# Optimization experiments

Hardware: AMD Instinct MI355X
Metric: run time of the kernel (lower is better)

Reference implementation:

```python
import jax, jax.numpy as jnp
import numpy as np

N = 16384
DIM_IN = 128
DIM_OUT = 128
HIDDEN = (DIM_IN + DIM_OUT) // 2  # 128


def setup_inputs() -> dict:
    key = jax.random.key(0)
    ks = jax.random.split(key, 8)
    s_in = 1.0 / np.sqrt(DIM_IN)
    s_h = 1.0 / np.sqrt(HIDDEN)
    return {
        "x": jax.random.normal(ks[0], (N, DIM_IN), dtype=jnp.float32),
        "adj": jax.random.uniform(ks[1], (N, N), dtype=jnp.float32) * (1.0 / N),
        "W2": jax.random.uniform(ks[2], (DIM_IN, HIDDEN), minval=-s_in, maxval=s_in, dtype=jnp.float32),
        "b2": jnp.zeros((HIDDEN,), dtype=jnp.float32),
        "W4": jax.random.uniform(ks[3], (HIDDEN, DIM_OUT), minval=-s_h, maxval=s_h, dtype=jnp.float32),
        "b4": jnp.zeros((DIM_OUT,), dtype=jnp.float32),
        "res_w": jax.random.uniform(ks[4], (DIM_OUT, HIDDEN), minval=-s_h, maxval=s_h, dtype=jnp.float32),
        "res_b": jax.random.uniform(ks[5], (DIM_OUT,), minval=-s_h, maxval=s_h, dtype=jnp.float32),
    }


def gcn(x, adj, W, b):
    # GraphConvolution: support = x @ W; out = adj @ support + b
    return adj @ (x @ W) + b


def reference(x, adj, W2, b2, W4, b4, res_w, res_b):
    local_hidden = gcn(x, adj, W2, b2)          # [N, HIDDEN]
    local_cross = gcn(local_hidden, adj, W4, b4)  # [N, DIM_OUT]
    # addRes: residual linear projection of local_hidden
    embed = local_cross + local_hidden @ res_w.T + res_b
    return embed
```

## Files before the change

kernel.cpp:

```cpp
#include <hip/hip_runtime.h>
#include <hip/hip_bf16.h>

#define MN 16384
#define SPLITS 4
#define KSLICE (MN / SPLITS)
#define BK 64
#define NSTEPS (KSLICE / BK)
#define NSUPER (NSTEPS / 2)

typedef float f32x4 __attribute__((ext_vector_type(4)));
typedef int   i32x4 __attribute__((ext_vector_type(4)));

#define A8S 32768.0f
#define SB1 64.0f
#define SB2 4096.0f
#define SC1 (1.0f / (32768.0f * 64.0f))
#define SC2 (1.0f / (32768.0f * 4096.0f))

__device__ __forceinline__ void async16(void* lds, const void* g) {
  __builtin_amdgcn_global_load_lds(
      (const __attribute__((address_space(1))) unsigned int*)g,
      (__attribute__((address_space(3))) unsigned int*)lds, 16, 0, 0);
}


__global__ __launch_bounds__(256)
void k1_xw2(const float* __restrict__ x, const float* __restrict__ W2,
            unsigned char* __restrict__ B1) {
  __shared__ __align__(16) float xs[64 * 128];
  const int t = threadIdx.x;
  const long rowbase = (long)blockIdx.x * 64;
  const f32x4* xg = (const f32x4*)(x + rowbase * 128);
  f32x4* xl = (f32x4*)xs;
#pragma unroll
  for (int i = 0; i < 8; ++i) xl[t + 256 * i] = xg[t + 256 * i];
  __syncthreads();
  const int r0 = (t >> 5) * 8;
  const int c0 = (t & 31) * 4;
  float acc[8][4] = {};
  for (int k = 0; k < 128; k += 4) {
    f32x4 w[4];
#pragma unroll
    for (int kk = 0; kk < 4; ++kk) w[kk] = *(const f32x4*)(W2 + (k + kk) * 128 + c0);
#pragma unroll
    for (int i = 0; i < 8; ++i) {
      f32x4 xv = *(const f32x4*)(xs + (r0 + i) * 128 + k);
#pragma unroll
      for (int kk = 0; kk < 4; ++kk)
#pragma unroll
        for (int j = 0; j < 4; ++j) acc[i][j] += xv[kk] * w[kk][j];
    }
  }
  const long U = (rowbase + r0) >> 3;
  i32x4 wv0, wv1;
#pragma unroll
  for (int j = 0; j < 4; ++j) {
    int lo = __builtin_amdgcn_cvt_pk_fp8_f32(acc[0][j] * SB1, acc[1][j] * SB1, 0, false);
    lo     = __builtin_amdgcn_cvt_pk_fp8_f32(acc[2][j] * SB1, acc[3][j] * SB1, lo, true);
    int hi = __builtin_amdgcn_cvt_pk_fp8_f32(acc[4][j] * SB1, acc[5][j] * SB1, 0, false);
    hi     = __builtin_amdgcn_cvt_pk_fp8_f32(acc[6][j] * SB1, acc[7][j] * SB1, hi, true);
    if (j < 2) { wv0[2 * j] = lo; wv0[2 * j + 1] = hi; }
    else       { wv1[2 * (j - 2)] = lo; wv1[2 * (j - 2) + 1] = hi; }
  }
  *(i32x4*)(B1 + (U * 128 + c0) * 8)      = wv0;
  *(i32x4*)(B1 + (U * 128 + c0) * 8 + 16) = wv1;
}

template <int AMODE>
__global__ __launch_bounds__(256, 4)
void big_mm(const float* __restrict__ A, const unsigned char* __restrict__ A8r,
            unsigned char* __restrict__ A8w, const unsigned char* __restrict__ B8,
            float sc, float* __restrict__ P) {
  __shared__ __align__(16) unsigned char Bs[2][16384];
  const int tid  = threadIdx.x;
  const int wid  = tid >> 6;
  const int lane = tid & 63;
  const int g    = lane >> 4;
  const int cl   = lane & 15;
  const int tile_m = blockIdx.x & 255;
  const int s      = blockIdx.x >> 8;
  const long k0 = (long)s * KSLICE;

  const char* bsrc = (const char*)B8 + k0 * 128 + (long)tid * 16;
  const float* aptr = nullptr;
  if constexpr (AMODE != 1)
    aptr = A + (long)(tile_m * 64 + wid * 16 + cl) * MN + k0 + 16 * g;
  const long c8base = (long)blockIdx.x * (64L * 4096) + (long)tid * 16;

  f32x4 acc[8] = {};

  {
    unsigned char* d = &Bs[0][0] + wid * 1024;
    async16(d, bsrc);                 async16(d + 4096, bsrc + 4096);
    async16(d + 8192, bsrc + 8192);   async16(d + 12288, bsrc + 12288);
  }
  f32x4 a0n, a1n, a2n, a3n;
  i32x4 q8n;
  if constexpr (AMODE == 1) {
    q8n = *(const i32x4*)(A8r + c8base);
  } else {
    a0n = *(const f32x4*)aptr;       a1n = *(const f32x4*)(aptr + 4);
    a2n = *(const f32x4*)(aptr + 8); a3n = *(const f32x4*)(aptr + 12);
  }
  __syncthreads();

  for (int m = 0; m < NSUPER; ++m) {
    if (m + 1 < NSUPER) {
      unsigned char* d = &Bs[(m + 1) & 1][0] + wid * 1024;
      const char* src = bsrc + (long)(2 * m + 2) * 8192;
      async16(d, src);                 async16(d + 4096, src + 4096);
      async16(d + 8192, src + 8192);   async16(d + 12288, src + 12288);
    }
    __builtin_amdgcn_sched_barrier(0);

#pragma unroll
    for (int h = 0; h < 2; ++h) {
      const int t = 2 * m + h;
      int pk0, pk1, pk2, pk3;
      if constexpr (AMODE == 1) {
        i32x4 q8 = q8n;
        if (t + 1 < NSTEPS)
          q8n = *(const i32x4*)(A8r + c8base + (long)(t + 1) * 4096);
        pk0 = q8[0]; pk1 = q8[1]; pk2 = q8[2]; pk3 = q8[3];
      } else {
        f32x4 a0 = a0n, a1 = a1n, a2 = a2n, a3 = a3n;
        if (t + 1 < NSTEPS) {
          const float* ap = aptr + (long)(t + 1) * BK;
          a0n = *(const f32x4*)ap;       a1n = *(const f32x4*)(ap + 4);
          a2n = *(const f32x4*)(ap + 8); a3n = *(const f32x4*)(ap + 12);
        }
        pk0 = __builtin_amdgcn_cvt_pk_fp8_f32(a0[0] * A8S, a0[1] * A8S, 0, false);
        pk0 = __builtin_amdgcn_cvt_pk_fp8_f32(a0[2] * A8S, a0[3] * A8S, pk0, true);
        pk1 = __builtin_amdgcn_cvt_pk_fp8_f32(a1[0] * A8S, a1[1] * A8S, 0, false);
        pk1 = __builtin_amdgcn_cvt_pk_fp8_f32(a1[2] * A8S, a1[3] * A8S, pk1, true);
        pk2 = __builtin_amdgcn_cvt_pk_fp8_f32(a2[0] * A8S, a2[1] * A8S, 0, false);
        pk2 = __builtin_amdgcn_cvt_pk_fp8_f32(a2[2] * A8S, a2[3] * A8S, pk2, true);
        pk3 = __builtin_amdgcn_cvt_pk_fp8_f32(a3[0] * A8S, a3[1] * A8S, 0, false);
        pk3 = __builtin_amdgcn_cvt_pk_fp8_f32(a3[2] * A8S, a3[3] * A8S, pk3, true);
        if constexpr (AMODE == 0) {
          i32x4 st = {pk0, pk1, pk2, pk3};
          __builtin_nontemporal_store(st, (i32x4*)(A8w + c8base + (long)t * 4096));
        }
      }
      const long alo = ((long)(unsigned)pk1 << 32) | (unsigned)pk0;
      const long ahi = ((long)(unsigned)pk3 << 32) | (unsigned)pk2;

      const char* bb = (const char*)&Bs[m & 1][0] + h * 8192 + g * 2048 + cl * 8;
#pragma unroll
      for (int c = 0; c < 8; ++c) {
        long b0 = *(const long*)(bb + c * 128);
        long b1 = *(const long*)(bb + 1024 + c * 128);
        acc[c] = __builtin_amdgcn_mfma_f32_16x16x32_fp8_fp8(alo, b0, acc[c], 0, 0, 0);
        acc[c] = __builtin_amdgcn_mfma_f32_16x16x32_fp8_fp8(ahi, b1, acc[c], 0, 0, 0);
      }
    }

    if (m + 1 < NSUPER) {
      if constexpr (AMODE == 0)      asm volatile("s_waitcnt vmcnt(10)" ::: "memory");
      else if constexpr (AMODE == 2) asm volatile("s_waitcnt vmcnt(8)" ::: "memory");
      else                           asm volatile("s_waitcnt vmcnt(2)" ::: "memory");
      __builtin_amdgcn_s_barrier();
    }
  }

  float* pb = P + ((long)s * MN + tile_m * 64 + wid * 16) * 128;
#pragma unroll
  for (int c = 0; c < 8; ++c)
#pragma unroll
    for (int q = 0; q < 4; ++q)
      __builtin_nontemporal_store(acc[c][q] * sc,
                                  &pb[(g * 4 + q) * 128 + 16 * c + cl]);
}

__global__ __launch_bounds__(256)
void k3_mid(const float* __restrict__ P, const float* __restrict__ b2,
            const float* __restrict__ W4, const float* __restrict__ res_w,
            const float* __restrict__ b4, const float* __restrict__ res_b,
            unsigned char* __restrict__ B2, float* __restrict__ Rr) {
  __shared__ __align__(16) float hs[64 * 128];
  const int t = threadIdx.x;
  const long rowbase = (long)blockIdx.x * 64;
  const long base = rowbase * 32;
  const f32x4* P0 = (const f32x4*)P + base;
  const f32x4* P1 = (const f32x4*)P + (long)MN * 32 + base;
  const f32x4* P2 = (const f32x4*)P + 2L * MN * 32 + base;
  const f32x4* P3 = (const f32x4*)P + 3L * MN * 32 + base;
  const f32x4* b2v = (const f32x4*)b2;
  f32x4* hl = (f32x4*)hs;
#pragma unroll
  for (int i = 0; i < 8; ++i) {
    int idx = t + 256 * i;
    f32x4 v = __builtin_nontemporal_load(P0 + idx);
    v += __builtin_nontemporal_load(P1 + idx);
    v += __builtin_nontemporal_load(P2 + idx);
    v += __builtin_nontemporal_load(P3 + idx);
    hl[idx] = v + b2v[idx & 31];
  }
  __syncthreads();
  const int r0 = (t >> 5) * 8;
  const int c0 = (t & 31) * 4;
  float acc2[8][4] = {};
  float accR[8][4] = {};
  for (int k = 0; k < 128; k += 4) {
    f32x4 w4v[4], rwv[4];
#pragma unroll
    for (int kk = 0; kk < 4; ++kk) w4v[kk] = *(const f32x4*)(W4 + (k + kk) * 128 + c0);
#pragma unroll
    for (int j = 0; j < 4; ++j) rwv[j] = *(const f32x4*)(res_w + (c0 + j) * 128 + k);
#pragma unroll
    for (int i = 0; i < 8; ++i) {
      f32x4 xv = *(const f32x4*)(hs + (r0 + i) * 128 + k);
#pragma unroll
      for (int kk = 0; kk < 4; ++kk)
#pragma unroll
        for (int j = 0; j < 4; ++j) {
          acc2[i][j] += xv[kk] * w4v[kk][j];
          accR[i][j] += xv[kk] * rwv[j][kk];
        }
    }
  }
  const long U = (rowbase + r0) >> 3;
  i32x4 wv0, wv1;
#pragma unroll
  for (int j = 0; j < 4; ++j) {
    int lo = __builtin_amdgcn_cvt_pk_fp8_f32(acc2[0][j] * SB2, acc2[1][j] * SB2, 0, false);
    lo     = __builtin_amdgcn_cvt_pk_fp8_f32(acc2[2][j] * SB2, acc2[3][j] * SB2, lo, true);
    int hi = __builtin_amdgcn_cvt_pk_fp8_f32(acc2[4][j] * SB2, acc2[5][j] * SB2, 0, false);
    hi     = __builtin_amdgcn_cvt_pk_fp8_f32(acc2[6][j] * SB2, acc2[7][j] * SB2, hi, true);
    if (j < 2) { wv0[2 * j] = lo; wv0[2 * j + 1] = hi; }
    else       { wv1[2 * (j - 2)] = lo; wv1[2 * (j - 2) + 1] = hi; }
  }
  *(i32x4*)(B2 + (U * 128 + c0) * 8)      = wv0;
  *(i32x4*)(B2 + (U * 128 + c0) * 8 + 16) = wv1;

  const f32x4 b4v = *(const f32x4*)(b4 + c0);
  const f32x4 rbv = *(const f32x4*)(res_b + c0);
#pragma unroll
  for (int i = 0; i < 8; ++i) {
    f32x4 rv;
#pragma unroll
    for (int j = 0; j < 4; ++j) rv[j] = accR[i][j];
    rv += b4v + rbv;
    *(f32x4*)(Rr + (rowbase + r0 + i) * 128 + c0) = rv;
  }
}

__global__ __launch_bounds__(256)
void k5_out(const float* __restrict__ P, const float* __restrict__ Rr,
            float* __restrict__ out) {
  const long i = (long)blockIdx.x * 256 + threadIdx.x;
  const f32x4* P0 = (const f32x4*)P;
  const f32x4* P1 = P0 + (long)MN * 32;
  const f32x4* P2 = P0 + 2L * MN * 32;
  const f32x4* P3 = P0 + 3L * MN * 32;
  f32x4 v = __builtin_nontemporal_load(P0 + i);
  v += __builtin_nontemporal_load(P1 + i);
  v += __builtin_nontemporal_load(P2 + i);
  v += __builtin_nontemporal_load(P3 + i);
  v += *((const f32x4*)Rr + i);
  __builtin_nontemporal_store(v, (f32x4*)out + i);
}

extern "C" void kernel_launch(void* const* d_in, const int* in_sizes, int n_in,
                              void* d_out, int out_size, void* d_ws, size_t ws_size,
                              hipStream_t stream) {
  const float* x     = (const float*)d_in[0];
  const float* adj   = (const float*)d_in[1];
  const float* W2    = (const float*)d_in[2];
  const float* b2    = (const float*)d_in[3];
  const float* W4    = (const float*)d_in[4];
  const float* b4    = (const float*)d_in[5];
  const float* res_w = (const float*)d_in[6];
  const float* res_b = (const float*)d_in[7];
  float* out = (float*)d_out;

  char* ws = (char*)d_ws;
  unsigned char* B1 = (unsigned char*)ws;
  unsigned char* B2 = (unsigned char*)(ws + (4L << 20));
  float* Rr = (float*)(ws + (8L << 20));
  float* P  = (float*)(ws + (16L << 20));
  unsigned char* A8 = (unsigned char*)(ws + (48L << 20));

  const size_t need = (48L << 20) + (size_t)MN * MN;
  const bool fp8_copy = ws_size >= need;

  k1_xw2<<<dim3(256), dim3(256), 0, stream>>>(x, W2, B1);
  if (fp8_copy) {
    big_mm<0><<<dim3(256 * SPLITS), dim3(256), 0, stream>>>(adj, nullptr, A8, B1, SC1, P);
    k3_mid<<<dim3(256), dim3(256), 0, stream>>>(P, b2, W4, res_w, b4, res_b, B2, Rr);
    big_mm<1><<<dim3(256 * SPLITS), dim3(256), 0, stream>>>(nullptr, A8, nullptr, B2, SC2, P);
  } else {
    big_mm<2><<<dim3(256 * SPLITS), dim3(256), 0, stream>>>(adj, nullptr, nullptr, B1, SC1, P);
    k3_mid<<<dim3(256), dim3(256), 0, stream>>>(P, b2, W4, res_w, b4, res_b, B2, Rr);
    big_mm<2><<<dim3(256 * SPLITS), dim3(256), 0, stream>>>(adj, nullptr, nullptr, B2, SC2, P);
  }
  k5_out<<<dim3(2048), dim3(256), 0, stream>>>(P, Rr, out);
}
```

Measured before the change: 429.9 us.

## Use 1024-thread blocks holding the whole B slice in LDS, with fp8 split-K partials

Restructures big_mm so each 1024-thread block loads its entire 128KB B k-slice into LDS once and covers 256 rows. The 16 waves walk the k-steps in staggered order, which removes the double-buffered pipeline and its per-step barriers. The split count rises from 4 to 16, and the partial sums are stored as fp8 bytes instead of fp32, then dequantized and summed in k3_mid and k5_out. The aim is fewer barriers and less partial-sum traffic. The cost is extra fp8 rounding error on the partials, byte-granular scattered stores, and only one 128KB-LDS block resident per CU.

```diff
diff --git a/kernel.cpp b/kernel.cpp
--- a/kernel.cpp
+++ b/kernel.cpp
@@ -2,20 +2,24 @@
 #include <hip/hip_bf16.h>
 
 #define MN 16384
-#define SPLITS 4
+#define SPLITS 16
 #define KSLICE (MN / SPLITS)
 #define BK 64
 #define NSTEPS (KSLICE / BK)
-#define NSUPER (NSTEPS / 2)
+#define TROWS 256
+#define PSLICE (MN * 128L)
 
 typedef float f32x4 __attribute__((ext_vector_type(4)));
+typedef float f32x2 __attribute__((ext_vector_type(2)));
 typedef int   i32x4 __attribute__((ext_vector_type(4)));
 
-#define A8S 32768.0f
-#define SB1 64.0f
-#define SB2 4096.0f
-#define SC1 (1.0f / (32768.0f * 64.0f))
-#define SC2 (1.0f / (32768.0f * 4096.0f))
+#define A8S  32768.0f
+#define SB1  64.0f
+#define SB2  4096.0f
+#define F1ST 0.0078125f
+#define F2ST 0.001953125f
+#define K3SC (1.0f / 16384.0f)
+#define K5SC (1.0f / 262144.0f)
 
 __device__ __forceinline__ void async16(void* lds, const void* g) {
   __builtin_amdgcn_global_load_lds(
@@ -67,134 +71,130 @@
 }
 
 template <int AMODE>
-__global__ __launch_bounds__(256, 4)
+__global__ __launch_bounds__(1024, 4)
 void big_mm(const float* __restrict__ A, const unsigned char* __restrict__ A8r,
             unsigned char* __restrict__ A8w, const unsigned char* __restrict__ B8,
-            float sc, float* __restrict__ P) {
-  __shared__ __align__(16) unsigned char Bs[2][16384];
+            float fstore, unsigned char* __restrict__ P8) {
+  __shared__ __align__(16) unsigned char Bs[131072];
   const int tid  = threadIdx.x;
   const int wid  = tid >> 6;
   const int lane = tid & 63;
   const int g    = lane >> 4;
   const int cl   = lane & 15;
-  const int tile_m = blockIdx.x & 255;
-  const int s      = blockIdx.x >> 8;
+  const int tile_m = blockIdx.x & 63;
+  const int s      = blockIdx.x >> 6;
   const long k0 = (long)s * KSLICE;
 
-  const char* bsrc = (const char*)B8 + k0 * 128 + (long)tid * 16;
+  {
+    const char* src = (const char*)B8 + (long)s * 131072 +
+                      (long)wid * 1024 + (long)lane * 16;
+    unsigned char* dst = Bs + wid * 1024;
+#pragma unroll
+    for (int r = 0; r < 8; ++r)
+      async16(dst + r * 16384, src + (long)r * 16384);
+  }
+
+  const int row = tile_m * TROWS + wid * 16 + cl;
   const float* aptr = nullptr;
-  if constexpr (AMODE != 1)
-    aptr = A + (long)(tile_m * 64 + wid * 16 + cl) * MN + k0 + 16 * g;
-  const long c8base = (long)blockIdx.x * (64L * 4096) + (long)tid * 16;
+  if constexpr (AMODE != 1) aptr = A + (long)row * MN + k0 + 16 * g;
+  const long c8base = (long)blockIdx.x * (NSTEPS * 16384L) + (long)tid * 16;
 
   f32x4 acc[8] = {};
 
-  {
-    unsigned char* d = &Bs[0][0] + wid * 1024;
-    async16(d, bsrc);                 async16(d + 4096, bsrc + 4096);
-    async16(d + 8192, bsrc + 8192);   async16(d + 12288, bsrc + 12288);
-  }
-  f32x4 a0n, a1n, a2n, a3n;
-  i32x4 q8n;
+  f32x4 ab[2][4];
+  i32x4 qb[2];
   if constexpr (AMODE == 1) {
-    q8n = *(const i32x4*)(A8r + c8base);
+    qb[0] = *(const i32x4*)(A8r + c8base + (long)(wid & 15) * 16384);
+    qb[1] = *(const i32x4*)(A8r + c8base + (long)((wid + 1) & 15) * 16384);
   } else {
-    a0n = *(const f32x4*)aptr;       a1n = *(const f32x4*)(aptr + 4);
-    a2n = *(const f32x4*)(aptr + 8); a3n = *(const f32x4*)(aptr + 12);
+    const float* p0 = aptr + (long)(wid & 15) * BK;
+    const float* p1 = aptr + (long)((wid + 1) & 15) * BK;
+#pragma unroll
+    for (int j = 0; j < 4; ++j) {
+      ab[0][j] = *(const f32x4*)(p0 + 4 * j);
+      ab[1][j] = *(const f32x4*)(p1 + 4 * j);
+    }
   }
   __syncthreads();
 
-  for (int m = 0; m < NSUPER; ++m) {
-    if (m + 1 < NSUPER) {
-      unsigned char* d = &Bs[(m + 1) & 1][0] + wid * 1024;
-      const char* src = bsrc + (long)(2 * m + 2) * 8192;
-      async16(d, src);                 async16(d + 4096, src + 4096);
-      async16(d + 8192, src + 8192);   async16(d + 12288, src + 12288);
-    }
-    __builtin_amdgcn_sched_barrier(0);
-
-#pragma unroll
-    for (int h = 0; h < 2; ++h) {
-      const int t = 2 * m + h;
-      int pk0, pk1, pk2, pk3;
-      if constexpr (AMODE == 1) {
-        i32x4 q8 = q8n;
-        if (t + 1 < NSTEPS)
-          q8n = *(const i32x4*)(A8r + c8base + (long)(t + 1) * 4096);
-        pk0 = q8[0]; pk1 = q8[1]; pk2 = q8[2]; pk3 = q8[3];
-      } else {
-        f32x4 a0 = a0n, a1 = a1n, a2 = a2n, a3 = a3n;
-        if (t + 1 < NSTEPS) {
-          const float* ap = aptr + (long)(t + 1) * BK;
-          a0n = *(const f32x4*)ap;       a1n = *(const f32x4*)(ap + 4);
-          a2n = *(const f32x4*)(ap + 8); a3n = *(const f32x4*)(ap + 12);
-        }
-        pk0 = __builtin_amdgcn_cvt_pk_fp8_f32(a0[0] * A8S, a0[1] * A8S, 0, false);
-        pk0 = __builtin_amdgcn_cvt_pk_fp8_f32(a0[2] * A8S, a0[3] * A8S, pk0, true);
-        pk1 = __builtin_amdgcn_cvt_pk_fp8_f32(a1[0] * A8S, a1[1] * A8S, 0, false);
-        pk1 = __builtin_amdgcn_cvt_pk_fp8_f32(a1[2] * A8S, a1[3] * A8S, pk1, true);
-        pk2 = __builtin_amdgcn_cvt_pk_fp8_f32(a2[0] * A8S, a2[1] * A8S, 0, false);
-        pk2 = __builtin_amdgcn_cvt_pk_fp8_f32(a2[2] * A8S, a2[3] * A8S, pk2, true);
-        pk3 = __builtin_amdgcn_cvt_pk_fp8_f32(a3[0] * A8S, a3[1] * A8S, 0, false);
-        pk3 = __builtin_amdgcn_cvt_pk_fp8_f32(a3[2] * A8S, a3[3] * A8S, pk3, true);
-        if constexpr (AMODE == 0) {
-          i32x4 st = {pk0, pk1, pk2, pk3};
-          __builtin_nontemporal_store(st, (i32x4*)(A8w + c8base + (long)t * 4096));
-        }
+#pragma unroll
+  for (int i = 0; i < NSTEPS; ++i) {
+    const int t = (wid + i) & 15;
+    int pk0, pk1, pk2, pk3;
+    if constexpr (AMODE == 1) {
+      i32x4 q = qb[i & 1];
+      if (i + 2 < NSTEPS)
+        qb[i & 1] = *(const i32x4*)(A8r + c8base + (long)((wid + i + 2) & 15) * 16384);
+      pk0 = q[0]; pk1 = q[1]; pk2 = q[2]; pk3 = q[3];
+    } else {
+      f32x4 a0 = ab[i & 1][0], a1 = ab[i & 1][1], a2 = ab[i & 1][2], a3 = ab[i & 1][3];
+      if (i + 2 < NSTEPS) {
+        const float* ap = aptr + (long)((wid + i + 2) & 15) * BK;
+#pragma unroll
+        for (int j = 0; j < 4; ++j) ab[i & 1][j] = *(const f32x4*)(ap + 4 * j);
       }
-      const long alo = ((long)(unsigned)pk1 << 32) | (unsigned)pk0;
-      const long ahi = ((long)(unsigned)pk3 << 32) | (unsigned)pk2;
-
-      const char* bb = (const char*)&Bs[m & 1][0] + h * 8192 + g * 2048 + cl * 8;
-#pragma unroll
-      for (int c = 0; c < 8; ++c) {
-        long b0 = *(const long*)(bb + c * 128);
-        long b1 = *(const long*)(bb + 1024 + c * 128);
-        acc[c] = __builtin_amdgcn_mfma_f32_16x16x32_fp8_fp8(alo, b0, acc[c], 0, 0, 0);
-        acc[c] = __builtin_amdgcn_mfma_f32_16x16x32_fp8_fp8(ahi, b1, acc[c], 0, 0, 0);
+      pk0 = __builtin_amdgcn_cvt_pk_fp8_f32(a0[0] * A8S, a0[1] * A8S, 0, false);
+      pk0 = __builtin_amdgcn_cvt_pk_fp8_f32(a0[2] * A8S, a0[3] * A8S, pk0, true);
+      pk1 = __builtin_amdgcn_cvt_pk_fp8_f32(a1[0] * A8S, a1[1] * A8S, 0, false);
+      pk1 = __builtin_amdgcn_cvt_pk_fp8_f32(a1[2] * A8S, a1[3] * A8S, pk1, true);
+      pk2 = __builtin_amdgcn_cvt_pk_fp8_f32(a2[0] * A8S, a2[1] * A8S, 0, false);
+      pk2 = __builtin_amdgcn_cvt_pk_fp8_f32(a2[2] * A8S, a2[3] * A8S, pk2, true);
+      pk3 = __builtin_amdgcn_cvt_pk_fp8_f32(a3[0] * A8S, a3[1] * A8S, 0, false);
+      pk3 = __builtin_amdgcn_cvt_pk_fp8_f32(a3[2] * A8S, a3[3] * A8S, pk3, true);
+      if constexpr (AMODE == 0) {
+        i32x4 st = {pk0, pk1, pk2, pk3};
+        *(i32x4*)(A8w + c8base + (long)t * 16384) = st;
       }
     }
-
-    if (m + 1 < NSUPER) {
-      if constexpr (AMODE == 0)      asm volatile("s_waitcnt vmcnt(10)" ::: "memory");
-      else if constexpr (AMODE == 2) asm volatile("s_waitcnt vmcnt(8)" ::: "memory");
-      else                           asm volatile("s_waitcnt vmcnt(2)" ::: "memory");
-      __builtin_amdgcn_s_barrier();
-    }
-  }
-
-  float* pb = P + ((long)s * MN + tile_m * 64 + wid * 16) * 128;
-#pragma unroll
-  for (int c = 0; c < 8; ++c)
+    const long alo = ((long)(unsigned)pk1 << 32) | (unsigned)pk0;
+    const long ahi = ((long)(unsigned)pk3 << 32) | (unsigned)pk2;
+
+    const char* bb = (const char*)Bs + t * 8192 + g * 2048 + cl * 8;
+#pragma unroll
+    for (int c = 0; c < 8; ++c) {
+      long b0 = *(const long*)(bb + c * 128);
+      long b1 = *(const long*)(bb + 1024 + c * 128);
+      acc[c] = __builtin_amdgcn_mfma_f32_16x16x32_fp8_fp8(alo, b0, acc[c], 0, 0, 0);
+      acc[c] = __builtin_amdgcn_mfma_f32_16x16x32_fp8_fp8(ahi, b1, acc[c], 0, 0, 0);
+    }
+  }
+
+  unsigned char* pb = P8 + (long)s * PSLICE +
+                      (long)(tile_m * TROWS + wid * 16) * 128 + cl;
+#pragma unroll
+  for (int c = 0; c < 8; ++c) {
+    int w0 = __builtin_amdgcn_cvt_pk_fp8_f32(acc[c][0] * fstore, acc[c][1] * fstore, 0, false);
+    w0     = __builtin_amdgcn_cvt_pk_fp8_f32(acc[c][2] * fstore, acc[c][3] * fstore, w0, true);
 #pragma unroll
     for (int q = 0; q < 4; ++q)
-      __builtin_nontemporal_store(acc[c][q] * sc,
-                                  &pb[(g * 4 + q) * 128 + 16 * c + cl]);
+      __builtin_nontemporal_store((unsigned char)(((unsigned)w0) >> (8 * q)),
+                                  pb + (g * 4 + q) * 128 + 16 * c);
+  }
 }
 
 __global__ __launch_bounds__(256)
-void k3_mid(const float* __restrict__ P, const float* __restrict__ b2,
+void k3_mid(const unsigned char* __restrict__ P8, const float* __restrict__ b2,
             const float* __restrict__ W4, const float* __restrict__ res_w,
             const float* __restrict__ b4, const float* __restrict__ res_b,
             unsigned char* __restrict__ B2, float* __restrict__ Rr) {
   __shared__ __align__(16) float hs[64 * 128];
   const int t = threadIdx.x;
   const long rowbase = (long)blockIdx.x * 64;
-  const long base = rowbase * 32;
-  const f32x4* P0 = (const f32x4*)P + base;
-  const f32x4* P1 = (const f32x4*)P + (long)MN * 32 + base;
-  const f32x4* P2 = (const f32x4*)P + 2L * MN * 32 + base;
-  const f32x4* P3 = (const f32x4*)P + 3L * MN * 32 + base;
   const f32x4* b2v = (const f32x4*)b2;
   f32x4* hl = (f32x4*)hs;
 #pragma unroll
   for (int i = 0; i < 8; ++i) {
-    int idx = t + 256 * i;
-    f32x4 v = __builtin_nontemporal_load(P0 + idx);
-    v += __builtin_nontemporal_load(P1 + idx);
-    v += __builtin_nontemporal_load(P2 + idx);
-    v += __builtin_nontemporal_load(P3 + idx);
-    hl[idx] = v + b2v[idx & 31];
+    const int idx = t + 256 * i;
+    const unsigned char* pp = P8 + rowbase * 128 + (long)idx * 4;
+    f32x4 v = {};
+#pragma unroll
+    for (int sl = 0; sl < SPLITS; ++sl) {
+      unsigned q = *(const unsigned*)(pp + (long)sl * PSLICE);
+      f32x2 lo = __builtin_amdgcn_cvt_pk_f32_fp8(q, false);
+      f32x2 hi = __builtin_amdgcn_cvt_pk_f32_fp8(q, true);
+      v[0] += lo[0]; v[1] += lo[1]; v[2] += hi[0]; v[3] += hi[1];
+    }
+    hl[idx] = v * K3SC + b2v[idx & 31];
   }
   __syncthreads();
   const int r0 = (t >> 5) * 8;
@@ -246,18 +246,19 @@
 }
 
 __global__ __launch_bounds__(256)
-void k5_out(const float* __restrict__ P, const float* __restrict__ Rr,
+void k5_out(const unsigned char* __restrict__ P8, const float* __restrict__ Rr,
             float* __restrict__ out) {
   const long i = (long)blockIdx.x * 256 + threadIdx.x;
-  const f32x4* P0 = (const f32x4*)P;
-  const f32x4* P1 = P0 + (long)MN * 32;
-  const f32x4* P2 = P0 + 2L * MN * 32;
-  const f32x4* P3 = P0 + 3L * MN * 32;
-  f32x4 v = __builtin_nontemporal_load(P0 + i);
-  v += __builtin_nontemporal_load(P1 + i);
-  v += __builtin_nontemporal_load(P2 + i);
-  v += __builtin_nontemporal_load(P3 + i);
-  v += *((const f32x4*)Rr + i);
+  const unsigned char* pp = P8 + i * 4;
+  f32x4 v = {};
+#pragma unroll
+  for (int sl = 0; sl < SPLITS; ++sl) {
+    unsigned q = *(const unsigned*)(pp + (long)sl * PSLICE);
+    f32x2 lo = __builtin_amdgcn_cvt_pk_f32_fp8(q, false);
+    f32x2 hi = __builtin_amdgcn_cvt_pk_f32_fp8(q, true);
+    v[0] += lo[0]; v[1] += lo[1]; v[2] += hi[0]; v[3] += hi[1];
+  }
+  v = v * K5SC + *((const f32x4*)Rr + i);
   __builtin_nontemporal_store(v, (f32x4*)out + i);
 }
 
@@ -275,24 +276,25 @@
   float* out = (float*)d_out;
 
   char* ws = (char*)d_ws;
-  unsigned char* B1 = (unsigned char*)ws;
-  unsigned char* B2 = (unsigned char*)(ws + (4L << 20));
-  float* Rr = (float*)(ws + (8L << 20));
-  float* P  = (float*)(ws + (16L << 20));
-  unsigned char* A8 = (unsigned char*)(ws + (48L << 20));
-
-  const size_t need = (48L << 20) + (size_t)MN * MN;
+  unsigned char* P8 = (unsigned char*)ws;
+  unsigned char* B1 = (unsigned char*)(ws + (32L << 20));
+  unsigned char* B2 = (unsigned char*)(ws + (34L << 20));
+  float* Rr = (float*)(ws + (36L << 20));
+  unsigned char* A8 = (unsigned char*)(ws + (44L << 20));
+
+  const size_t need = (44L << 20) + (size_t)MN * MN;
   const bool fp8_copy = ws_size >= need;
 
+  const int BIGGRID = SPLITS * (MN / TROWS);
   k1_xw2<<<dim3(256), dim3(256), 0, stream>>>(x, W2, B1);
   if (fp8_copy) {
-    big_mm<0><<<dim3(256 * SPLITS), dim3(256), 0, stream>>>(adj, nullptr, A8, B1, SC1, P);
-    k3_mid<<<dim3(256), dim3(256), 0, stream>>>(P, b2, W4, res_w, b4, res_b, B2, Rr);
-    big_mm<1><<<dim3(256 * SPLITS), dim3(256), 0, stream>>>(nullptr, A8, nullptr, B2, SC2, P);
+    big_mm<0><<<dim3(BIGGRID), dim3(1024), 0, stream>>>(adj, nullptr, A8, B1, F1ST, P8);
+    k3_mid<<<dim3(256), dim3(256), 0, stream>>>(P8, b2, W4, res_w, b4, res_b, B2, Rr);
+    big_mm<1><<<dim3(BIGGRID), dim3(1024), 0, stream>>>(nullptr, A8, nullptr, B2, F2ST, P8);
   } else {
-    big_mm<2><<<dim3(256 * SPLITS), dim3(256), 0, stream>>>(adj, nullptr, nullptr, B1, SC1, P);
-    k3_mid<<<dim3(256), dim3(256), 0, stream>>>(P, b2, W4, res_w, b4, res_b, B2, Rr);
-    big_mm<2><<<dim3(256 * SPLITS), dim3(256), 0, stream>>>(adj, nullptr, nullptr, B2, SC2, P);
-  }
-  k5_out<<<dim3(2048), dim3(256), 0, stream>>>(P, Rr, out);
-}
+    big_mm<2><<<dim3(BIGGRID), dim3(1024), 0, stream>>>(adj, nullptr, nullptr, B1, F1ST, P8);
+    k3_mid<<<dim3(256), dim3(256), 0, stream>>>(P8, b2, W4, res_w, b4, res_b, B2, Rr);
+    big_mm<2><<<dim3(BIGGRID), dim3(1024), 0, stream>>>(adj, nullptr, nullptr, B2, F2ST, P8);
+  }
+  k5_out<<<dim3(2048), dim3(256), 0, stream>>>(P8, Rr, out);
+}
```

After: 497.7 us. +15.8%, slower.

## Stage fp32 adjacency tiles through swizzled LDS with async loads, 128-row blocks

Applied to the files above, without the earlier changes.

The big adjacency matmul now uses 512-thread blocks covering 128 rows each, which halves the grid. The fp32 A tile is streamed into a double-buffered, XOR-swizzled LDS region with async global-to-LDS loads instead of direct register loads. The loop is flattened to single 64-wide k-steps with one barrier per step, and the B staging shrinks to one 8KB buffer per step. The aim is to get wider, better-coalesced A reads that overlap with MFMA work. The cost is 80KB of LDS per block, which lowers occupancy, plus twice as many barriers.

```diff
diff --git a/kernel.cpp b/kernel.cpp
--- a/kernel.cpp
+++ b/kernel.cpp
@@ -6,7 +6,6 @@
 #define KSLICE (MN / SPLITS)
 #define BK 64
 #define NSTEPS (KSLICE / BK)
-#define NSUPER (NSTEPS / 2)
 
 typedef float f32x4 __attribute__((ext_vector_type(4)));
 typedef int   i32x4 __attribute__((ext_vector_type(4)));
@@ -67,103 +66,111 @@
 }
 
 template <int AMODE>
-__global__ __launch_bounds__(256, 4)
+__global__ __launch_bounds__(512, 4)
 void big_mm(const float* __restrict__ A, const unsigned char* __restrict__ A8r,
             unsigned char* __restrict__ A8w, const unsigned char* __restrict__ B8,
             float sc, float* __restrict__ P) {
-  __shared__ __align__(16) unsigned char Bs[2][16384];
+  constexpr int LDSSZ = (AMODE == 1) ? 16384 : 81920;
+  __shared__ __align__(16) unsigned char LB[LDSSZ];
   const int tid  = threadIdx.x;
   const int wid  = tid >> 6;
   const int lane = tid & 63;
   const int g    = lane >> 4;
   const int cl   = lane & 15;
-  const int tile_m = blockIdx.x & 255;
-  const int s      = blockIdx.x >> 8;
+  const int tile_m = blockIdx.x & 127;
+  const int s      = blockIdx.x >> 7;
   const long k0 = (long)s * KSLICE;
 
   const char* bsrc = (const char*)B8 + k0 * 128 + (long)tid * 16;
-  const float* aptr = nullptr;
-  if constexpr (AMODE != 1)
-    aptr = A + (long)(tile_m * 64 + wid * 16 + cl) * MN + k0 + 16 * g;
-  const long c8base = (long)blockIdx.x * (64L * 4096) + (long)tid * 16;
+  const long c8base = (long)blockIdx.x * (64L * 8192) + (long)tid * 16;
+
+  const char* asrc[4];
+  int aoff[4];
+  if constexpr (AMODE != 1) {
+    const int rl = lane >> 4;
+#pragma unroll
+    for (int q = 0; q < 4; ++q) {
+      const int row_local = wid * 16 + q * 4 + rl;
+      const int piece = ((lane & 15) * 16) ^ ((row_local & 7) << 4);
+      asrc[q] = (const char*)A + ((long)(tile_m * 128 + row_local) * MN + k0) * 4 + piece;
+    }
+    const int row = wid * 16 + cl;
+#pragma unroll
+    for (int j = 0; j < 4; ++j)
+      aoff[j] = 16384 + row * 256 + ((g * 64 + j * 16) ^ ((cl & 7) << 4));
+  }
 
   f32x4 acc[8] = {};
 
-  {
-    unsigned char* d = &Bs[0][0] + wid * 1024;
-    async16(d, bsrc);                 async16(d + 4096, bsrc + 4096);
-    async16(d + 8192, bsrc + 8192);   async16(d + 12288, bsrc + 12288);
-  }
-  f32x4 a0n, a1n, a2n, a3n;
+  if constexpr (AMODE != 1) {
+#pragma unroll
+    for (int q = 0; q < 4; ++q)
+      async16(LB + 16384 + (wid * 4 + q) * 1024, asrc[q]);
+  }
+  async16(LB + wid * 1024, bsrc);
   i32x4 q8n;
-  if constexpr (AMODE == 1) {
-    q8n = *(const i32x4*)(A8r + c8base);
-  } else {
-    a0n = *(const f32x4*)aptr;       a1n = *(const f32x4*)(aptr + 4);
-    a2n = *(const f32x4*)(aptr + 8); a3n = *(const f32x4*)(aptr + 12);
-  }
+  if constexpr (AMODE == 1) q8n = *(const i32x4*)(A8r + c8base);
   __syncthreads();
 
-  for (int m = 0; m < NSUPER; ++m) {
-    if (m + 1 < NSUPER) {
-      unsigned char* d = &Bs[(m + 1) & 1][0] + wid * 1024;
-      const char* src = bsrc + (long)(2 * m + 2) * 8192;
-      async16(d, src);                 async16(d + 4096, src + 4096);
-      async16(d + 8192, src + 8192);   async16(d + 12288, src + 12288);
+  for (int t = 0; t < NSTEPS; ++t) {
+    const int bank = t & 1;
+    if (t + 1 < NSTEPS) {
+      const int nb = bank ^ 1;
+      if constexpr (AMODE != 1) {
+#pragma unroll
+        for (int q = 0; q < 4; ++q)
+          async16(LB + 16384 + nb * 32768 + (wid * 4 + q) * 1024,
+                  asrc[q] + (long)(t + 1) * 256);
+      }
+      async16(LB + nb * 8192 + wid * 1024, bsrc + (long)(t + 1) * 8192);
     }
     __builtin_amdgcn_sched_barrier(0);
 
-#pragma unroll
-    for (int h = 0; h < 2; ++h) {
-      const int t = 2 * m + h;
-      int pk0, pk1, pk2, pk3;
-      if constexpr (AMODE == 1) {
-        i32x4 q8 = q8n;
-        if (t + 1 < NSTEPS)
-          q8n = *(const i32x4*)(A8r + c8base + (long)(t + 1) * 4096);
-        pk0 = q8[0]; pk1 = q8[1]; pk2 = q8[2]; pk3 = q8[3];
-      } else {
-        f32x4 a0 = a0n, a1 = a1n, a2 = a2n, a3 = a3n;
-        if (t + 1 < NSTEPS) {
-          const float* ap = aptr + (long)(t + 1) * BK;
-          a0n = *(const f32x4*)ap;       a1n = *(const f32x4*)(ap + 4);
-          a2n = *(const f32x4*)(ap + 8); a3n = *(const f32x4*)(ap + 12);
-        }
-        pk0 = __builtin_amdgcn_cvt_pk_fp8_f32(a0[0] * A8S, a0[1] * A8S, 0, false);
-        pk0 = __builtin_amdgcn_cvt_pk_fp8_f32(a0[2] * A8S, a0[3] * A8S, pk0, true);
-        pk1 = __builtin_amdgcn_cvt_pk_fp8_f32(a1[0] * A8S, a1[1] * A8S, 0, false);
-        pk1 = __builtin_amdgcn_cvt_pk_fp8_f32(a1[2] * A8S, a1[3] * A8S, pk1, true);
-        pk2 = __builtin_amdgcn_cvt_pk_fp8_f32(a2[0] * A8S, a2[1] * A8S, 0, false);
-        pk2 = __builtin_amdgcn_cvt_pk_fp8_f32(a2[2] * A8S, a2[3] * A8S, pk2, true);
-        pk3 = __builtin_amdgcn_cvt_pk_fp8_f32(a3[0] * A8S, a3[1] * A8S, 0, false);
-        pk3 = __builtin_amdgcn_cvt_pk_fp8_f32(a3[2] * A8S, a3[3] * A8S, pk3, true);
-        if constexpr (AMODE == 0) {
-          i32x4 st = {pk0, pk1, pk2, pk3};
-          __builtin_nontemporal_store(st, (i32x4*)(A8w + c8base + (long)t * 4096));
-        }
+    int pk0, pk1, pk2, pk3;
+    if constexpr (AMODE == 1) {
+      i32x4 q8 = q8n;
+      if (t + 1 < NSTEPS)
+        q8n = *(const i32x4*)(A8r + c8base + (long)(t + 1) * 8192);
+      pk0 = q8[0]; pk1 = q8[1]; pk2 = q8[2]; pk3 = q8[3];
+    } else {
+      f32x4 ar0 = *(const f32x4*)(LB + bank * 32768 + aoff[0]);
+      f32x4 ar1 = *(const f32x4*)(LB + bank * 32768 + aoff[1]);
+      f32x4 ar2 = *(const f32x4*)(LB + bank * 32768 + aoff[2]);
+      f32x4 ar3 = *(const f32x4*)(LB + bank * 32768 + aoff[3]);
+      pk0 = __builtin_amdgcn_cvt_pk_fp8_f32(ar0[0] * A8S, ar0[1] * A8S, 0, false);
+      pk0 = __builtin_amdgcn_cvt_pk_fp8_f32(ar0[2] * A8S, ar0[3] * A8S, pk0, true);
+      pk1 = __builtin_amdgcn_cvt_pk_fp8_f32(ar1[0] * A8S, ar1[1] * A8S, 0, false);
+      pk1 = __builtin_amdgcn_cvt_pk_fp8_f32(ar1[2] * A8S, ar1[3] * A8S, pk1, true);
+      pk2 = __builtin_amdgcn_cvt_pk_fp8_f32(ar2[0] * A8S, ar2[1] * A8S, 0, false);
+      pk2 = __builtin_amdgcn_cvt_pk_fp8_f32(ar2[2] * A8S, ar2[3] * A8S, pk2, true);
+      pk3 = __builtin_amdgcn_cvt_pk_fp8_f32(ar3[0] * A8S, ar3[1] * A8S, 0, false);
+      pk3 = __builtin_amdgcn_cvt_pk_fp8_f32(ar3[2] * A8S, ar3[3] * A8S, pk3, true);
+      if constexpr (AMODE == 0) {
+        i32x4 st = {pk0, pk1, pk2, pk3};
+        __builtin_nontemporal_store(st, (i32x4*)(A8w + c8base + (long)t * 8192));
       }
-      const long alo = ((long)(unsigned)pk1 << 32) | (unsigned)pk0;
-      const long ahi = ((long)(unsigned)pk3 << 32) | (unsigned)pk2;
-
-      const char* bb = (const char*)&Bs[m & 1][0] + h * 8192 + g * 2048 + cl * 8;
-#pragma unroll
-      for (int c = 0; c < 8; ++c) {
-        long b0 = *(const long*)(bb + c * 128);
-        long b1 = *(const long*)(bb + 1024 + c * 128);
-        acc[c] = __builtin_amdgcn_mfma_f32_16x16x32_fp8_fp8(alo, b0, acc[c], 0, 0, 0);
-        acc[c] = __builtin_amdgcn_mfma_f32_16x16x32_fp8_fp8(ahi, b1, acc[c], 0, 0, 0);
-      }
-    }
-
-    if (m + 1 < NSUPER) {
-      if constexpr (AMODE == 0)      asm volatile("s_waitcnt vmcnt(10)" ::: "memory");
-      else if constexpr (AMODE == 2) asm volatile("s_waitcnt vmcnt(8)" ::: "memory");
-      else                           asm volatile("s_waitcnt vmcnt(2)" ::: "memory");
+    }
+    const long alo = ((long)(unsigned)pk1 << 32) | (unsigned)pk0;
+    const long ahi = ((long)(unsigned)pk3 << 32) | (unsigned)pk2;
+
+    const char* bb = (const char*)LB + bank * 8192 + g * 2048 + cl * 8;
+#pragma unroll
+    for (int c = 0; c < 8; ++c) {
+      long b0 = *(const long*)(bb + c * 128);
+      long b1 = *(const long*)(bb + 1024 + c * 128);
+      acc[c] = __builtin_amdgcn_mfma_f32_16x16x32_fp8_fp8(alo, b0, acc[c], 0, 0, 0);
+      acc[c] = __builtin_amdgcn_mfma_f32_16x16x32_fp8_fp8(ahi, b1, acc[c], 0, 0, 0);
+    }
+
+    if (t + 1 < NSTEPS) {
+      if constexpr (AMODE == 0)      asm volatile("s_waitcnt vmcnt(1)" ::: "memory");
+      else if constexpr (AMODE == 2) asm volatile("s_waitcnt vmcnt(0)" ::: "memory");
+      else                           asm volatile("s_waitcnt vmcnt(1)" ::: "memory");
       __builtin_amdgcn_s_barrier();
     }
   }
 
-  float* pb = P + ((long)s * MN + tile_m * 64 + wid * 16) * 128;
+  float* pb = P + ((long)s * MN + tile_m * 128 + wid * 16) * 128;
 #pragma unroll
   for (int c = 0; c < 8; ++c)
 #pragma unroll
@@ -286,13 +293,13 @@
 
   k1_xw2<<<dim3(256), dim3(256), 0, stream>>>(x, W2, B1);
   if (fp8_copy) {
-    big_mm<0><<<dim3(256 * SPLITS), dim3(256), 0, stream>>>(adj, nullptr, A8, B1, SC1, P);
+    big_mm<0><<<dim3(128 * SPLITS), dim3(512), 0, stream>>>(adj, nullptr, A8, B1, SC1, P);
     k3_mid<<<dim3(256), dim3(256), 0, stream>>>(P, b2, W4, res_w, b4, res_b, B2, Rr);
-    big_mm<1><<<dim3(256 * SPLITS), dim3(256), 0, stream>>>(nullptr, A8, nullptr, B2, SC2, P);
+    big_mm<1><<<dim3(128 * SPLITS), dim3(512), 0, stream>>>(nullptr, A8, nullptr, B2, SC2, P);
   } else {
-    big_mm<2><<<dim3(256 * SPLITS), dim3(256), 0, stream>>>(adj, nullptr, nullptr, B1, SC1, P);
+    big_mm<2><<<dim3(128 * SPLITS), dim3(512), 0, stream>>>(adj, nullptr, nullptr, B1, SC1, P);
     k3_mid<<<dim3(256), dim3(256), 0, stream>>>(P, b2, W4, res_w, b4, res_b, B2, Rr);
-    big_mm<2><<<dim3(256 * SPLITS), dim3(256), 0, stream>>>(adj, nullptr, nullptr, B2, SC2, P);
+    big_mm<2><<<dim3(128 * SPLITS), dim3(512), 0, stream>>>(adj, nullptr, nullptr, B2, SC2, P);
   }
   k5_out<<<dim3(2048), dim3(256), 0, stream>>>(P, Rr, out);
 }
```

Result: no change. 422.2 us (-1.8%).
